# Kernel tuning notes

Measured on AMD Instinct MI355X. Metric: run time of the kernel, lower is better.

## Reference

```python
import jax, jax.numpy as jnp
import numpy as np
import math

B, T, D_MODEL, N_HEADS = 4, 2048, 1024, 16
HEAD_DIM = D_MODEL // N_HEADS


def setup_inputs() -> dict:
    key = jax.random.key(0)
    k1, k2, k3 = jax.random.split(key, 3)
    x = jax.random.normal(k1, (B, T, D_MODEL), dtype=jnp.float32)
    # torch Linear weight layout: [out_features, in_features]
    w_qkv = jax.random.normal(k2, (3 * D_MODEL, D_MODEL), dtype=jnp.float32) * (1.0 / math.sqrt(D_MODEL))
    w_out = jax.random.normal(k3, (D_MODEL, D_MODEL), dtype=jnp.float32) * (1.0 / math.sqrt(D_MODEL))
    return {"x": x, "w_qkv": w_qkv, "w_out": w_out}


def reference(x, w_qkv, w_out):
    b, t, c = x.shape
    h, d = N_HEADS, HEAD_DIM
    # qkv projection: (B,T,3C) -> (3,B,H,T,D)
    qkv = jnp.einsum('btc,fc->btf', x, w_qkv)
    qkv = qkv.reshape(b, t, 3, h, d).transpose(2, 0, 3, 1, 4)
    q, k, v = qkv[0], qkv[1], qkv[2]
    scale = 1.0 / math.sqrt(d)
    # full O(T^2) attention scores, causal masked
    scores = jnp.einsum('bhqd,bhkd->bhqk', q, k) * scale
    causal = jnp.tril(jnp.ones((t, t), dtype=bool))
    scores = jnp.where(causal[None, None, :, :], scores, jnp.float32(-jnp.inf))
    attn = jax.nn.softmax(scores, axis=-1)
    out = jnp.einsum('bhqk,bhkd->bhqd', attn, v)  # (B,H,T,D)
    out = out.transpose(0, 2, 1, 3).reshape(b, t, c)
    out = jnp.einsum('btc,oc->bto', out, w_out)
    return out
```

## Files before the change

kernel.cpp:

```cpp
#include <hip/hip_runtime.h>
#include <hip/hip_bf16.h>

#define T_SEQ 2048
#define BATCH 4
#define NH    16
#define DM    1024
#define HD    64

typedef __attribute__((ext_vector_type(4))) float  f32x4;
typedef __attribute__((ext_vector_type(8))) short  s16x8;
typedef __attribute__((ext_vector_type(4))) short  s16x4;

__device__ __forceinline__ unsigned short f2b(float f) {
  union { float f; unsigned u; } v; v.f = f;
  unsigned u = v.u;
  unsigned r = 0x7fffu + ((u >> 16) & 1u);
  u += r;
  return (unsigned short)(u >> 16);
}

__device__ __forceinline__ f32x4 mfma16(s16x8 a, s16x8 b, f32x4 c) {
  return __builtin_amdgcn_mfma_f32_16x16x32_bf16(a, b, c, 0, 0, 0);
}

__device__ __forceinline__ float exp2_fast(float x) {
  float r; asm("v_exp_f32 %0, %1" : "=v"(r) : "v"(x)); return r;
}

__device__ __forceinline__ unsigned cvt_pk_bf16(float lo, float hi) {
  unsigned r; asm("v_cvt_pk_bf16_f32 %0, %1, %2" : "=v"(r) : "v"(lo), "v"(hi)); return r;
}

#define BAR() __builtin_amdgcn_s_barrier()
#define SCB() __builtin_amdgcn_sched_barrier(0)
#define LGK(n) do { asm volatile("s_waitcnt lgkmcnt(" #n ")" ::: "memory"); SCB(); } while (0)
#define VMC(n) do { asm volatile("s_waitcnt vmcnt(" #n ")" ::: "memory"); } while (0)

__global__ void cvt_all(const float* __restrict__ x, const float* __restrict__ wq,
                        const float* __restrict__ wo,
                        unsigned short* __restrict__ xb, unsigned short* __restrict__ wqb,
                        unsigned short* __restrict__ wob) {
  const int N4X = (BATCH * T_SEQ * DM) / 4;
  const int N4Q = (3 * DM * DM) / 4;
  const int N4O = (DM * DM) / 4;
  const int N4QSCALED = (DM * DM) / 4;
  int i = blockIdx.x * blockDim.x + threadIdx.x;
  int stride = gridDim.x * blockDim.x;
  for (int j = i; j < N4X + N4Q + N4O; j += stride) {
    const float* src; unsigned short* dst; int k; float scale = 1.f;
    if (j < N4X) { src = x; dst = xb; k = j; }
    else if (j < N4X + N4Q) {
      k = j - N4X; src = wq; dst = wqb;
      if (k < N4QSCALED) scale = 0.18033688011112042f;
    } else { k = j - N4X - N4Q; src = wo; dst = wob; }
    f32x4 v = ((const f32x4*)src)[k];
    s16x4 o;
    o.x = (short)f2b(v.x * scale); o.y = (short)f2b(v.y * scale);
    o.z = (short)f2b(v.z * scale); o.w = (short)f2b(v.w * scale);
    ((s16x4*)dst)[k] = o;
  }
}

__device__ __forceinline__ void rd4(s16x8 (&d)[4], const char* base, int rbase, int cb) {
#pragma unroll
  for (int j = 0; j < 4; ++j)
    d[j] = *(const s16x8*)(base + (rbase + j * 16) * 128 + cb);
}

__device__ __forceinline__ void stage_half(const unsigned short* __restrict__ Msrc,
                                           int rt0, int kt, char* lbase, int half,
                                           int srow8, int c2src, int c2lin, int Kd) {
#pragma unroll
  for (int q = 0; q < 2; ++q) {
    int rl = half * 128 + q * 64 + srow8;
    const char* src = (const char*)(Msrc + (size_t)(rt0 + rl) * Kd + kt) + c2src;
    __builtin_amdgcn_global_load_lds((const void*)src, (void*)(lbase + rl * 128 + c2lin),
                                     16, 0, 0);
  }
}

__device__ __forceinline__ void clust(f32x4 (&acc)[8][4], const s16x8 (&a)[4],
                                      const s16x8 (&b)[4], int mb) {
  __builtin_amdgcn_s_setprio(1);
#pragma unroll
  for (int j = 0; j < 4; ++j)
#pragma unroll
    for (int n = 0; n < 4; ++n)
      acc[mb + j][n] = mfma16(a[j], b[n], acc[mb + j][n]);
  __builtin_amdgcn_s_setprio(0);
}

__global__ __launch_bounds__(512, 2)
void gemm8p(const unsigned short* __restrict__ A, const unsigned short* __restrict__ B,
            unsigned short* __restrict__ C, int M, int N, int K) {
  __shared__ char smem[131072];
  char* A0b = smem;
  char* A1b = smem + 32768;
  char* B0b = smem + 65536;
  char* B1b = smem + 98304;

  const int tid = threadIdx.x;
  const int lane = tid & 63;
  const int w = tid >> 6;
  const int wm = w >> 2, wn = w & 3;
  const int lr = lane & 15, g = lane >> 4;

  const int gx = gridDim.x, nwg = gx * gridDim.y;
  const int bid = blockIdx.y * gx + blockIdx.x;
  const int cpx = nwg >> 3;
  const int b2 = (bid & 7) * cpx + (bid >> 3);
  const int row0 = (b2 % gx) * 256;
  const int col0 = (b2 / gx) * 256;

  const int srow8 = tid >> 3;
  const int c2lin = (tid & 7) * 16;
  const int swzS = ((srow8 & 4) << 3) | ((srow8 & 8) << 1);
  const int c2src = c2lin ^ swzS;

  const int swzL = ((lr & 4) << 3) | ((lr & 8) << 1);
  const int cs0 = (g * 16) ^ swzL;
  const int cs1 = 64 + cs0;
  const int rAlo = wm * 128 + lr;
  const int rAhi = rAlo + 64;
  const int rB = wn * 64 + lr;

  f32x4 acc[8][4] = {};
  s16x8 aP[4], aQ[4], aR[4], bP[4], bQ[4];

  const int NITER = K / 128;
  const int ktLast = K - 64;

  stage_half(A, row0, 0, A0b, 0, srow8, c2src, c2lin, K);
  stage_half(A, row0, 0, A0b, 1, srow8, c2src, c2lin, K);
  stage_half(B, col0, 0, B0b, 0, srow8, c2src, c2lin, K);
  stage_half(B, col0, 0, B0b, 1, srow8, c2src, c2lin, K);
  stage_half(A, row0, 64, A1b, 0, srow8, c2src, c2lin, K);
  VMC(2);
  BAR();
  rd4(aP, A0b, rAlo, cs0);
  rd4(bP, B0b, rB, cs0);

  for (int it = 0; it < NITER; ++it) {
    const int ktO = it * 128 + 64;
    const int kt2 = min(it * 128 + 128, ktLast);
    const int kt3 = min(it * 128 + 192, ktLast);

    rd4(aQ, A0b, rAhi, cs0);
    stage_half(B, col0, ktO, B1b, 0, srow8, c2src, c2lin, K);
    BAR(); LGK(4);
    clust(acc, aP, bP, 0);
    BAR();
    rd4(aP, A0b, rAlo, cs1);
    rd4(aR, A0b, rAhi, cs1);
    rd4(bQ, B0b, rB, cs1);
    stage_half(B, col0, ktO, B1b, 1, srow8, c2src, c2lin, K);
    BAR(); LGK(12);
    clust(acc, aQ, bP, 4);
    BAR();
    stage_half(A, row0, ktO, A1b, 1, srow8, c2src, c2lin, K);
    BAR(); LGK(0);
    clust(acc, aP, bQ, 0);
    BAR();
    stage_half(A, row0, kt2, A0b, 0, srow8, c2src, c2lin, K);
    VMC(2);
    BAR();
    rd4(aP, A1b, rAlo, cs0);
    rd4(bP, B1b, rB, cs0);
    clust(acc, aR, bQ, 4);
    BAR();
    rd4(aQ, A1b, rAhi, cs0);
    stage_half(B, col0, kt2, B0b, 0, srow8, c2src, c2lin, K);
    BAR(); LGK(4);
    clust(acc, aP, bP, 0);
    BAR();
    rd4(aP, A1b, rAlo, cs1);
    rd4(aR, A1b, rAhi, cs1);
    rd4(bQ, B1b, rB, cs1);
    stage_half(B, col0, kt2, B0b, 1, srow8, c2src, c2lin, K);
    BAR(); LGK(12);
    clust(acc, aQ, bP, 4);
    BAR();
    stage_half(A, row0, kt2, A0b, 1, srow8, c2src, c2lin, K);
    BAR(); LGK(0);
    clust(acc, aP, bQ, 0);
    BAR();
    stage_half(A, row0, kt3, A1b, 0, srow8, c2src, c2lin, K);
    VMC(2);
    BAR();
    rd4(aP, A0b, rAlo, cs0);
    rd4(bP, B0b, rB, cs0);
    clust(acc, aR, bQ, 4);
    BAR();
  }

#pragma unroll
  for (int m = 0; m < 8; ++m)
#pragma unroll
    for (int n = 0; n < 4; ++n)
#pragma unroll
      for (int i = 0; i < 4; ++i) {
        int row = row0 + wm * 128 + m * 16 + g * 4 + i;
        int col = col0 + wn * 64 + n * 16 + lr;
        C[(size_t)row * N + col] = f2b(acc[m][n][i]);
      }
}

template<int OUT_F32>
__global__ __launch_bounds__(256)
void gemm_bt(const unsigned short* __restrict__ A,
             const unsigned short* __restrict__ B,
             void* __restrict__ C, int M, int N, int K) {
  __shared__ unsigned short As[128 * 32];
  __shared__ unsigned short Bs[128 * 32];
  const int tid  = threadIdx.x;
  const int lane = tid & 63;
  const int w    = tid >> 6;
  const int wr   = w >> 1, wc = w & 1;
  const int lr   = lane & 15, g = lane >> 4;

  const int gx  = gridDim.x, nwg = gx * gridDim.y;
  const int bid = blockIdx.y * gx + blockIdx.x;
  const int cpx = nwg >> 3;
  const int b2  = (bid & 7) * cpx + (bid >> 3);
  const int row0 = (b2 % gx) * 128;
  const int col0 = (b2 / gx) * 128;

  const int srow = w * 16 + (lane >> 2);
  const int scol = (lane & 3) * 8;

  f32x4 acc[4][4] = {};

  for (int kt = 0; kt < K; kt += 32) {
    __syncthreads();
#pragma unroll
    for (int s = 0; s < 2; ++s) {
      const unsigned short* srcA = A + (size_t)(row0 + s * 64 + srow) * K + kt + scol;
      __builtin_amdgcn_global_load_lds((const void*)srcA, (void*)&As[(s * 64 + w * 16) * 32], 16, 0, 0);
      const unsigned short* srcB = B + (size_t)(col0 + s * 64 + srow) * K + kt + scol;
      __builtin_amdgcn_global_load_lds((const void*)srcB, (void*)&Bs[(s * 64 + w * 16) * 32], 16, 0, 0);
    }
    __syncthreads();

    s16x8 af[4], bf[4];
#pragma unroll
    for (int m = 0; m < 4; ++m)
      af[m] = *(const s16x8*)&As[(wr * 64 + m * 16 + lr) * 32 + g * 8];
#pragma unroll
    for (int n = 0; n < 4; ++n)
      bf[n] = *(const s16x8*)&Bs[(wc * 64 + n * 16 + lr) * 32 + g * 8];
#pragma unroll
    for (int m = 0; m < 4; ++m)
#pragma unroll
      for (int n = 0; n < 4; ++n)
        acc[m][n] = mfma16(af[m], bf[n], acc[m][n]);
  }

#pragma unroll
  for (int m = 0; m < 4; ++m)
#pragma unroll
    for (int n = 0; n < 4; ++n)
#pragma unroll
      for (int i = 0; i < 4; ++i) {
        int row = row0 + wr * 64 + m * 16 + g * 4 + i;
        int col = col0 + wc * 64 + n * 16 + lr;
        if (OUT_F32)
          ((float*)C)[(size_t)row * N + col] = acc[m][n][i];
        else
          ((unsigned short*)C)[(size_t)row * N + col] = f2b(acc[m][n][i]);
      }
}

__global__ __launch_bounds__(512)
void attn_kernel(const unsigned short* __restrict__ qkv,
                 unsigned short* __restrict__ out) {
  __shared__ unsigned short Ks[2][64 * 64];
  __shared__ unsigned short Vt[2][64 * 72];
  __shared__ unsigned short Ps[8][16 * 72];

  const int tid  = threadIdx.x;
  const int lane = tid & 63;
  const int w    = tid >> 6;
  const int lr   = lane & 15, g = lane >> 4;
  const int bid  = blockIdx.x;
  const int bh   = bid & 63;
  const int pi   = bid >> 6;
  const int b    = bh >> 4, h = bh & 15;
  const size_t rb = (size_t)b * T_SEQ;

  const bool grpV = (tid < 256);
  const int vd0 = (tid & 7) * 8, vr0 = (tid >> 3) * 2;
  const int t2  = tid - 256;
  const int kr0 = t2 >> 3, kc0 = t2 & 7;

#pragma unroll 1
  for (int ph = 0; ph < 2; ++ph) {
    const int qt = ph ? (15 - pi) : pi;
    const int q0 = qt * 128;
    const int qr = q0 + w * 16;
    const int qq = qr + lr;
    const int nt = 2 * qt + 2;
    const int qmax = qr + 15;

    s16x8 qf[2];
    {
      const unsigned short* qp = qkv + (rb + qq) * 3072 + h * 64;
      qf[0] = *(const s16x8*)(qp + g * 8);
      qf[1] = *(const s16x8*)(qp + 32 + g * 8);
    }

    float mI = -1e30f, lI = 0.f;
    f32x4 o[4] = {};

    s16x8 pre0, pre1;
    {
      if (grpV) {
        const unsigned short* vp = &qkv[(rb + vr0) * 3072 + 2048 + h * 64 + vd0];
        pre0 = *(const s16x8*)vp;
        pre1 = *(const s16x8*)(vp + 3072);
      } else {
        const unsigned short* kp = &qkv[(rb + kr0) * 3072 + 1024 + h * 64 + kc0 * 8];
        pre0 = *(const s16x8*)kp;
        pre1 = *(const s16x8*)(kp + 32 * 3072);
      }
    }

    for (int t = 0; t < nt; ++t) {
      const int cur = t & 1;
      if (grpV) {
#pragma unroll
        for (int jj = 0; jj < 8; ++jj) {
          int d = vd0 + jj;
          int sw = ((d ^ (d >> 3)) & 7) << 4;
          unsigned val = (unsigned)(unsigned short)pre0[jj] |
                         ((unsigned)(unsigned short)pre1[jj] << 16);
          *(unsigned*)((char*)&Vt[cur][0] + d * 144 + ((vr0 * 2) ^ sw)) = val;
        }
      } else {
        *(s16x8*)((char*)&Ks[cur][0] + kr0 * 128 + ((kc0 * 16) ^ ((kr0 & 7) << 4))) = pre0;
        int kr1 = kr0 + 32;
        *(s16x8*)((char*)&Ks[cur][0] + kr1 * 128 + ((kc0 * 16) ^ ((kr1 & 7) << 4))) = pre1;
      }
      __syncthreads();

      if (t + 1 < nt) {
        const int kv0n = (t + 1) * 64;
        if (grpV) {
          const unsigned short* vp = &qkv[(rb + kv0n + vr0) * 3072 + 2048 + h * 64 + vd0];
          pre0 = *(const s16x8*)vp;
          pre1 = *(const s16x8*)(vp + 3072);
        } else {
          const unsigned short* kp = &qkv[(rb + kv0n + kr0) * 3072 + 1024 + h * 64 + kc0 * 8];
          pre0 = *(const s16x8*)kp;
          pre1 = *(const s16x8*)(kp + 32 * 3072);
        }
      }

      const int kv0 = t * 64;
      if (kv0 <= qmax) {
        f32x4 s4[4];
        __builtin_amdgcn_s_setprio(1);
#pragma unroll
        for (int kc = 0; kc < 4; ++kc) {
          int row = kc * 16 + lr;
          const char* kbase = (const char*)&Ks[cur][0] + row * 128;
          int sw = (row & 7) << 4;
          s16x8 kf0 = *(const s16x8*)(kbase + ((g * 16) ^ sw));
          s16x8 kf1 = *(const s16x8*)(kbase + ((64 + g * 16) ^ sw));
          f32x4 s = {};
          s = mfma16(kf0, qf[0], s);
          s = mfma16(kf1, qf[1], s);
          s4[kc] = s;
        }
        __builtin_amdgcn_s_setprio(0);

        if (kv0 + 63 > qr) {
#pragma unroll
          for (int kc = 0; kc < 4; ++kc)
#pragma unroll
            for (int i = 0; i < 4; ++i) {
              int key = kv0 + kc * 16 + g * 4 + i;
              if (key > qq) s4[kc][i] = -1e30f;
            }
        }

        float mx = fmaxf(fmaxf(fmaxf(s4[0][0], s4[0][1]), fmaxf(s4[0][2], s4[0][3])),
                   fmaxf(fmaxf(fmaxf(s4[1][0], s4[1][1]), fmaxf(s4[1][2], s4[1][3])),
                   fmaxf(fmaxf(fmaxf(s4[2][0], s4[2][1]), fmaxf(s4[2][2], s4[2][3])),
                         fmaxf(fmaxf(s4[3][0], s4[3][1]), fmaxf(s4[3][2], s4[3][3])))));
        mx = fmaxf(mx, __shfl_xor(mx, 16));
        mx = fmaxf(mx, __shfl_xor(mx, 32));

        const bool defer = __all(mx - mI <= 11.5f);
        float alpha;
        if (defer) {
          alpha = 1.f;
        } else {
          float mn = fmaxf(mI, mx);
          alpha = exp2_fast(mI - mn);
          mI = mn;
        }
        float rs = 0.f;
#pragma unroll
        for (int kc = 0; kc < 4; ++kc)
#pragma unroll
          for (int i = 0; i < 4; ++i) {
            float p = exp2_fast(s4[kc][i] - mI);
            s4[kc][i] = p;
            rs += p;
          }
        rs += __shfl_xor(rs, 16);
        rs += __shfl_xor(rs, 32);
        lI = lI * alpha + rs;

        {
          char* pw = (char*)&Ps[w][0] + lr * 144;
#pragma unroll
          for (int kc = 0; kc < 4; ++kc) {
            unsigned v0 = cvt_pk_bf16(s4[kc][0], s4[kc][1]);
            unsigned v1 = cvt_pk_bf16(s4[kc][2], s4[kc][3]);
            unsigned long long pv = (unsigned long long)v0 | ((unsigned long long)v1 << 32);
            *(unsigned long long*)(pw + kc * 32 + g * 8) = pv;
          }
        }

        if (!defer) {
#pragma unroll
          for (int n = 0; n < 4; ++n)
#pragma unroll
            for (int i = 0; i < 4; ++i)
              o[n][i] *= alpha;
        }

        asm volatile("s_waitcnt lgkmcnt(0)" ::: "memory");

        __builtin_amdgcn_s_setprio(1);
#pragma unroll
        for (int kk = 0; kk < 2; ++kk) {
          s16x8 pf = *(const s16x8*)((const char*)&Ps[w][0] + lr * 144 + kk * 64 + g * 16);
#pragma unroll
          for (int n = 0; n < 4; ++n) {
            int d = n * 16 + lr;
            int sw = ((d ^ (d >> 3)) & 7) << 4;
            s16x8 vf = *(const s16x8*)((const char*)&Vt[cur][0] + d * 144 + ((kk * 64 + g * 16) ^ sw));
            o[n] = mfma16(vf, pf, o[n]);
          }
        }
        __builtin_amdgcn_s_setprio(0);
      }
    }

    float rl = 1.f / lI;
#pragma unroll
    for (int n = 0; n < 4; ++n) {
      unsigned p0 = cvt_pk_bf16(o[n][0] * rl, o[n][1] * rl);
      unsigned p1 = cvt_pk_bf16(o[n][2] * rl, o[n][3] * rl);
      unsigned long long pv = (unsigned long long)p0 | ((unsigned long long)p1 << 32);
      *(unsigned long long*)&out[(rb + qq) * 1024 + h * 64 + n * 16 + g * 4] = pv;
    }
  }
}

extern "C" void kernel_launch(void* const* d_in, const int* in_sizes, int n_in,
                              void* d_out, int out_size, void* d_ws, size_t ws_size,
                              hipStream_t stream) {
  const float* x     = (const float*)d_in[0];
  const float* w_qkv = (const float*)d_in[1];
  const float* w_out = (const float*)d_in[2];

  const size_t n_x   = (size_t)BATCH * T_SEQ * DM;
  const size_t n_wq  = (size_t)3 * DM * DM;
  const size_t n_wo  = (size_t)DM * DM;
  const size_t n_qkv = (size_t)BATCH * T_SEQ * 3 * DM;
  const size_t need  = (n_x + n_wq + n_wo + n_qkv + n_x) * 2;
  if (ws_size < need) return;

  unsigned short* xb  = (unsigned short*)d_ws;
  unsigned short* wqb = xb + n_x;
  unsigned short* wob = wqb + n_wq;
  unsigned short* qkv = wob + n_wo;
  unsigned short* att = qkv + n_qkv;

  cvt_all<<<2048, 256, 0, stream>>>(x, w_qkv, w_out, xb, wqb, wob);

  gemm8p<<<dim3(32, 12), 512, 0, stream>>>(xb, wqb, qkv, BATCH * T_SEQ, 3 * DM, DM);
  attn_kernel<<<512, 512, 0, stream>>>(qkv, att);
  gemm_bt<1><<<dim3(64, 8), 256, 0, stream>>>(att, wob, d_out, BATCH * T_SEQ, DM, DM);
}
```

Measured before the change: 199.3 us.

## Change LDS swizzle to XOR row bits and reorder stage prefetch schedule

Replaces the LDS swizzle, which used two row bits, with a full 3-bit XOR of the row index into the 16-byte column chunk, aiming to cut shared-memory bank conflicts on fragment reads. Also restructures the 256x256 GEMM main loop into a lambda body called with alternating buffers. It changes the order of the global-to-LDS staging so the next tile's A-high, B-low and B-high halves are issued earlier and the A-low half of the tile after that is prefetched. The schedule depends on the existing wait counts staying correct, which risks races or stalls if they no longer match.

After: 190.2 us. -4.6%, faster.

```diff
diff --git a/kernel.cpp b/kernel.cpp
--- a/kernel.cpp
+++ b/kernel.cpp
@@ -114,12 +114,11 @@
 
   const int srow8 = tid >> 3;
   const int c2lin = (tid & 7) * 16;
-  const int swzS = ((srow8 & 4) << 3) | ((srow8 & 8) << 1);
-  const int c2src = c2lin ^ swzS;
-
-  const int swzL = ((lr & 4) << 3) | ((lr & 8) << 1);
-  const int cs0 = (g * 16) ^ swzL;
-  const int cs1 = 64 + cs0;
+  const int c2src = ((tid & 7) ^ (srow8 & 7)) * 16;
+
+  const int swz = (lr & 7) << 4;
+  const int cs0 = (g * 16) ^ swz;
+  const int cs1 = (64 + g * 16) ^ swz;
   const int rAlo = wm * 128 + lr;
   const int rAhi = rAlo + 64;
   const int rB = wn * 64 + lr;
@@ -127,8 +126,7 @@
   f32x4 acc[8][4] = {};
   s16x8 aP[4], aQ[4], aR[4], bP[4], bQ[4];
 
-  const int NITER = K / 128;
-  const int ktLast = K - 64;
+  const int NT = K / 64;
 
   stage_half(A, row0, 0, A0b, 0, srow8, c2src, c2lin, K);
   stage_half(A, row0, 0, A0b, 1, srow8, c2src, c2lin, K);
@@ -140,57 +138,38 @@
   rd4(aP, A0b, rAlo, cs0);
   rd4(bP, B0b, rB, cs0);
 
-  for (int it = 0; it < NITER; ++it) {
-    const int ktO = it * 128 + 64;
-    const int kt2 = min(it * 128 + 128, ktLast);
-    const int kt3 = min(it * 128 + 192, ktLast);
-
-    rd4(aQ, A0b, rAhi, cs0);
-    stage_half(B, col0, ktO, B1b, 0, srow8, c2src, c2lin, K);
+  auto body = [&](char* Ac, char* Bc, char* An, char* Bn, int t) {
+    const int ktn  = min(t + 1, NT - 1) * 64;
+    const int ktn2 = min(t + 2, NT - 1) * 64;
+    rd4(aQ, Ac, rAhi, cs0);
+    stage_half(A, row0, ktn, An, 1, srow8, c2src, c2lin, K);
     BAR(); LGK(4);
     clust(acc, aP, bP, 0);
     BAR();
-    rd4(aP, A0b, rAlo, cs1);
-    rd4(aR, A0b, rAhi, cs1);
-    rd4(bQ, B0b, rB, cs1);
-    stage_half(B, col0, ktO, B1b, 1, srow8, c2src, c2lin, K);
+    rd4(aP, Ac, rAlo, cs1);
+    rd4(aR, Ac, rAhi, cs1);
+    rd4(bQ, Bc, rB, cs1);
+    stage_half(B, col0, ktn, Bn, 0, srow8, c2src, c2lin, K);
     BAR(); LGK(12);
     clust(acc, aQ, bP, 4);
     BAR();
-    stage_half(A, row0, ktO, A1b, 1, srow8, c2src, c2lin, K);
+    stage_half(B, col0, ktn, Bn, 1, srow8, c2src, c2lin, K);
     BAR(); LGK(0);
     clust(acc, aP, bQ, 0);
     BAR();
-    stage_half(A, row0, kt2, A0b, 0, srow8, c2src, c2lin, K);
+    stage_half(A, row0, ktn2, Ac, 0, srow8, c2src, c2lin, K);
     VMC(2);
     BAR();
-    rd4(aP, A1b, rAlo, cs0);
-    rd4(bP, B1b, rB, cs0);
+    rd4(aP, An, rAlo, cs0);
+    rd4(bP, Bn, rB, cs0);
     clust(acc, aR, bQ, 4);
     BAR();
-    rd4(aQ, A1b, rAhi, cs0);
-    stage_half(B, col0, kt2, B0b, 0, srow8, c2src, c2lin, K);
-    BAR(); LGK(4);
-    clust(acc, aP, bP, 0);
-    BAR();
-    rd4(aP, A1b, rAlo, cs1);
-    rd4(aR, A1b, rAhi, cs1);
-    rd4(bQ, B1b, rB, cs1);
-    stage_half(B, col0, kt2, B0b, 1, srow8, c2src, c2lin, K);
-    BAR(); LGK(12);
-    clust(acc, aQ, bP, 4);
-    BAR();
-    stage_half(A, row0, kt2, A0b, 1, srow8, c2src, c2lin, K);
-    BAR(); LGK(0);
-    clust(acc, aP, bQ, 0);
-    BAR();
-    stage_half(A, row0, kt3, A1b, 0, srow8, c2src, c2lin, K);
-    VMC(2);
-    BAR();
-    rd4(aP, A0b, rAlo, cs0);
-    rd4(bP, B0b, rB, cs0);
-    clust(acc, aR, bQ, 4);
-    BAR();
+  };
+
+#pragma unroll 1
+  for (int tt = 0; tt < NT; tt += 2) {
+    body(A0b, B0b, A1b, B1b, tt);
+    body(A1b, B1b, A0b, B0b, tt + 1);
   }
 
 #pragma unroll
```
